# Performance work log

Measured on AMD Instinct MI355X. Metric: run time of the kernel, lower is better.

## Reference

```python
import jax, jax.numpy as jnp
import numpy as np

VOCAB = 32000
HID = 1024
HEADS = 16
HEAD_DIM = HID // HEADS
LAYERS = 8
INTER = 4 * HID
ROPE_BASE = 100000.0
EPS = 1e-5


def setup_inputs() -> dict:
    key = jax.random.key(0)
    ks = jax.random.split(key, 12)
    s = 0.02
    inp = {
        'input_ids': jax.random.randint(ks[0], (2, 2048), 0, VOCAB),
        'embed_W': jax.random.normal(ks[1], (VOCAB, HID), jnp.float32) * s,
        'Wq': jax.random.normal(ks[2], (LAYERS, HID, HID), jnp.float32) * s,
        'Wk': jax.random.normal(ks[3], (LAYERS, HID, HID), jnp.float32) * s,
        'Wv': jax.random.normal(ks[4], (LAYERS, HID, HID), jnp.float32) * s,
        'Wo': jax.random.normal(ks[5], (LAYERS, HID, HID), jnp.float32) * s,
        'Wg': jax.random.normal(ks[6], (LAYERS, HID, INTER), jnp.float32) * s,
        'Wu': jax.random.normal(ks[7], (LAYERS, HID, INTER), jnp.float32) * s,
        'Wd': jax.random.normal(ks[8], (LAYERS, INTER, HID), jnp.float32) * s,
        'norm1_w': jnp.ones((LAYERS, HID), jnp.float32),
        'norm2_w': jnp.ones((LAYERS, HID), jnp.float32),
        'final_norm_w': jnp.ones((HID,), jnp.float32),
        'head_W': jax.random.normal(ks[9], (HID, VOCAB), jnp.float32) * s,
    }
    return inp


def rms_norm(x, w):
    return x * jax.lax.rsqrt(jnp.mean(x * x, axis=-1, keepdims=True) + EPS) * w


def rope_tables(seq_len):
    freq = 1.0 / (ROPE_BASE ** (jnp.arange(0, HEAD_DIM, 2, dtype=jnp.float32) / HEAD_DIM))
    ang = jnp.arange(seq_len, dtype=jnp.float32)[:, None] * freq  # [S, d/2]
    cos = jnp.concatenate([jnp.cos(ang), jnp.cos(ang)], axis=-1)  # [S, d]
    sin = jnp.concatenate([jnp.sin(ang), jnp.sin(ang)], axis=-1)
    return cos, sin


def rotate_half(x):
    h = x.shape[-1] // 2
    return jnp.concatenate([-x[..., h:], x[..., :h]], axis=-1)


def apply_rope(q, k, cos, sin):
    # q,k: [B,S,H,D]; cos,sin: [S,D] -> broadcast over heads via [:,None,:]
    c = cos[:, None, :]
    s = sin[:, None, :]
    return q * c + rotate_half(q) * s, k * c + rotate_half(k) * s


def attention(x, wq, wk, wv, wo, cos, sin, causal_mask):
    B, S, _ = x.shape
    q = (x @ wq).reshape(B, S, HEADS, HEAD_DIM)
    k = (x @ wk).reshape(B, S, HEADS, HEAD_DIM)
    v = (x @ wv).reshape(B, S, HEADS, HEAD_DIM)
    q, k = apply_rope(q, k, cos, sin)
    scores = jnp.einsum('bqhd,bkhd->bhqk', q, k) / np.sqrt(HEAD_DIM)
    scores = jnp.clip(scores, -1000.0, 1000.0)
    scores = jnp.where(causal_mask, jnp.finfo(scores.dtype).min, scores)
    w = jax.nn.softmax(scores.astype(jnp.float32), axis=-1).astype(q.dtype)
    w = jnp.clip(w, 0.0, 1.0)
    ctx = jnp.einsum('bhqk,bkhd->bqhd', w, v).reshape(B, S, HID)
    return ctx @ wo


def reference(input_ids, embed_W, Wq, Wk, Wv, Wo, Wg, Wu, Wd, norm1_w, norm2_w, final_norm_w, head_W):
    B, S = input_ids.shape
    h = embed_W[input_ids]  # [B,S,HID]
    cos, sin = rope_tables(S)
    causal_mask = jnp.triu(jnp.ones((S, S), bool), k=1)[None, None]
    for l in range(LAYERS):
        h = h + attention(rms_norm(h, norm1_w[l]), Wq[l], Wk[l], Wv[l], Wo[l], cos, sin, causal_mask)
        hn = rms_norm(h, norm2_w[l])
        h = h + (jax.nn.silu(hn @ Wg[l]) * (hn @ Wu[l])) @ Wd[l]
    h = rms_norm(h, final_norm_w)
    logits = h @ head_W
    return logits, h
```

## Files before the change

### kernel.cpp

```cpp
#include <hip/hip_runtime.h>

#define T_TOK 4096
#define SEQ   2048
#define HID   1024
#define NH    16
#define HD    64
#define INTER 4096
#define NLAYER 8
#define VOCAB 32000

typedef short short8 __attribute__((ext_vector_type(8)));
typedef float f32x4  __attribute__((ext_vector_type(4)));

__device__ __forceinline__ unsigned short f2bf(float f){
  unsigned int u = __builtin_bit_cast(unsigned int, f);
  u += 0x7fffu + ((u >> 16) & 1u);
  return (unsigned short)(u >> 16);
}
__device__ __forceinline__ float bf2f(unsigned short b){
  unsigned int u = ((unsigned int)b) << 16;
  return __builtin_bit_cast(float, u);
}

#define GLOAD_LDS16(gsrc, ldst) \
  __builtin_amdgcn_global_load_lds((const __attribute__((address_space(1))) void*)(gsrc), \
                                   (__attribute__((address_space(3))) void*)(ldst), 16, 0, 0)

__global__ __launch_bounds__(256) void embed_kernel(const int* __restrict__ ids,
                                                    const float* __restrict__ W,
                                                    float* __restrict__ h){
  int i = blockIdx.x * 256 + threadIdx.x;
  int t = i >> 8, c = i & 255;
  ((float4*)h)[i] = ((const float4*)(W + (size_t)ids[t] * HID))[c];
}

__global__ __launch_bounds__(256) void rope_tab_kernel(float* __restrict__ cosT,
                                                       float* __restrict__ sinT){
  int i = blockIdx.x * 256 + threadIdx.x;
  int s = i >> 5, f = i & 31;
  float inv = expf(-((2.0f * (float)f) / 64.0f) * logf(100000.0f));
  float ang = (float)s * inv;
  cosT[i] = cosf(ang);
  sinT[i] = sinf(ang);
}

__global__ __launch_bounds__(256) void rmsnorm_kernel(const float* __restrict__ h,
                                                      const float* __restrict__ w,
                                                      unsigned short* __restrict__ out,
                                                      float* hcopy){
  int t = blockIdx.x, tid = threadIdx.x;
  float4 v = ((const float4*)(h + (size_t)t * HID))[tid];
  float ss = v.x*v.x + v.y*v.y + v.z*v.z + v.w*v.w;
  #pragma unroll
  for (int m = 1; m < 64; m <<= 1) ss += __shfl_xor(ss, m);
  __shared__ float red[4];
  if ((tid & 63) == 0) red[tid >> 6] = ss;
  __syncthreads();
  float r = rsqrtf((red[0] + red[1] + red[2] + red[3]) * (1.0f / HID) + 1e-5f);
  float4 wv = ((const float4*)w)[tid];
  float nx = v.x * r * wv.x;
  float ny = v.y * r * wv.y;
  float nz = v.z * r * wv.z;
  float nw = v.w * r * wv.w;
  ushort4 o;
  o.x = f2bf(nx); o.y = f2bf(ny); o.z = f2bf(nz); o.w = f2bf(nw);
  ((ushort4*)(out + (size_t)t * HID))[tid] = o;
  if (hcopy){
    float4 hv; hv.x = nx; hv.y = ny; hv.z = nz; hv.w = nw;
    ((float4*)(hcopy + (size_t)t * HID))[tid] = hv;
  }
}

__global__ __launch_bounds__(256) void convert_w_qkvo(const float* __restrict__ W0,
                                                      const float* __restrict__ W1,
                                                      const float* __restrict__ W2,
                                                      const float* __restrict__ W3,
                                                      unsigned short* __restrict__ Wt){
  __shared__ unsigned short t_lds[64][72];
  const int z = blockIdx.z, sel = z >> 3, l = z & 7;
  const float* W = ((sel == 0) ? W0 : (sel == 1) ? W1 : (sel == 2) ? W2 : W3)
                 + (size_t)l * HID * HID;
  unsigned short* dst = Wt + (size_t)z * HID * HID;
  const int n0 = blockIdx.x * 64, k0 = blockIdx.y * 64;
  const int tid = threadIdx.x;
  const int tr = tid >> 4, tc = tid & 15;
  #pragma unroll
  for (int i = 0; i < 4; ++i){
    int kk = tr + i * 16;
    float4 v = *(const float4*)(W + (size_t)(k0 + kk) * HID + n0 + tc * 4);
    t_lds[tc*4+0][kk] = f2bf(v.x);
    t_lds[tc*4+1][kk] = f2bf(v.y);
    t_lds[tc*4+2][kk] = f2bf(v.z);
    t_lds[tc*4+3][kk] = f2bf(v.w);
  }
  __syncthreads();
  const int n = tid >> 2, cp = tid & 3;
  #pragma unroll
  for (int j = 0; j < 2; ++j){
    int c = cp * 2 + j;
    uint4 d = *(const uint4*)(&t_lds[n][c * 8]);
    *(uint4*)(dst + (size_t)(n0 + n) * HID + k0 + ((c ^ (n & 7)) << 3)) = d;
  }
}

__global__ __launch_bounds__(256) void convert_w_swz(const float* __restrict__ W,
                                                     unsigned short* __restrict__ Wt,
                                                     int K, int N){
  __shared__ unsigned short t_lds[64][72];
  W  += (size_t)blockIdx.z * K * N;
  Wt += (size_t)blockIdx.z * K * N;
  const int n0 = blockIdx.x * 64, k0 = blockIdx.y * 64;
  const int tid = threadIdx.x;
  const int tr = tid >> 4, tc = tid & 15;
  #pragma unroll
  for (int i = 0; i < 4; ++i){
    int kk = tr + i * 16;
    float4 v = *(const float4*)(W + (size_t)(k0 + kk) * N + n0 + tc * 4);
    t_lds[tc*4+0][kk] = f2bf(v.x);
    t_lds[tc*4+1][kk] = f2bf(v.y);
    t_lds[tc*4+2][kk] = f2bf(v.z);
    t_lds[tc*4+3][kk] = f2bf(v.w);
  }
  __syncthreads();
  const int n = tid >> 2, cp = tid & 3;
  #pragma unroll
  for (int j = 0; j < 2; ++j){
    int c = cp * 2 + j;
    uint4 d = *(const uint4*)(&t_lds[n][c * 8]);
    *(uint4*)(Wt + (size_t)(n0 + n) * K + k0 + ((c ^ (n & 7)) << 3)) = d;
  }
}

__global__ __launch_bounds__(256) void convert_w_lin(const float* __restrict__ W,
                                                     unsigned short* __restrict__ Wt,
                                                     int K, int N){
  __shared__ unsigned short t_lds[64][72];
  const int n0 = blockIdx.x * 64, k0 = blockIdx.y * 64;
  const int tid = threadIdx.x;
  const int tr = tid >> 4, tc = tid & 15;
  #pragma unroll
  for (int i = 0; i < 4; ++i){
    int kk = tr + i * 16;
    float4 v = *(const float4*)(W + (size_t)(k0 + kk) * N + n0 + tc * 4);
    t_lds[tc*4+0][kk] = f2bf(v.x);
    t_lds[tc*4+1][kk] = f2bf(v.y);
    t_lds[tc*4+2][kk] = f2bf(v.z);
    t_lds[tc*4+3][kk] = f2bf(v.w);
  }
  __syncthreads();
  const int n = tid >> 2, cp = tid & 3;
  #pragma unroll
  for (int j = 0; j < 2; ++j){
    int c = cp * 2 + j;
    uint4 d = *(const uint4*)(&t_lds[n][c * 8]);
    *(uint4*)(Wt + (size_t)(n0 + n) * K + k0 + c * 8) = d;
  }
}

__device__ __forceinline__ void gemm_core64(const unsigned short* __restrict__ A,
                                            const unsigned short* __restrict__ Bt,
                                            int K, int m0, int n0,
                                            unsigned short* As, unsigned short* Bs,
                                            f32x4 (&acc)[4][4]){
  const int tid = threadIdx.x;
  const int lane = tid & 63, w = tid >> 6;
  const int l15 = lane & 15, g = lane >> 4;
  const int lr = lane >> 3;
  const int lc = lane & 7;
  const int wr = w >> 1, wc = w & 1;
  const int axor = ((lc ^ lr) << 3);

  #pragma unroll
  for (int m = 0; m < 4; ++m)
    #pragma unroll
    for (int n = 0; n < 4; ++n)
      #pragma unroll
      for (int i = 0; i < 4; ++i) acc[m][n][i] = 0.0f;

  for (int kk = 0; kk < K; kk += 64){
    __syncthreads();
    #pragma unroll
    for (int i = 0; i < 4; ++i){
      int rb = (i * 4 + w) * 8;
      GLOAD_LDS16(A  + (size_t)(m0 + rb + lr) * K + kk + axor,      As + rb * 64);
      GLOAD_LDS16(Bt + (size_t)(n0 + rb + lr) * K + kk + (lc << 3), Bs + rb * 64);
    }
    __syncthreads();
    short8 a[4][2], b[4][2];
    const int x = l15 & 7;
    #pragma unroll
    for (int m = 0; m < 4; ++m){
      int row = wr * 64 + m * 16 + l15;
      a[m][0] = *(const short8*)(As + row * 64 + ((g       ^ x) << 3));
      a[m][1] = *(const short8*)(As + row * 64 + (((4 + g) ^ x) << 3));
    }
    #pragma unroll
    for (int n = 0; n < 4; ++n){
      int row = wc * 64 + n * 16 + l15;
      b[n][0] = *(const short8*)(Bs + row * 64 + ((g       ^ x) << 3));
      b[n][1] = *(const short8*)(Bs + row * 64 + (((4 + g) ^ x) << 3));
    }
    #pragma unroll
    for (int m = 0; m < 4; ++m)
      #pragma unroll
      for (int n = 0; n < 4; ++n){
        acc[m][n] = __builtin_amdgcn_mfma_f32_16x16x32_bf16(a[m][0], b[n][0], acc[m][n], 0, 0, 0);
        acc[m][n] = __builtin_amdgcn_mfma_f32_16x16x32_bf16(a[m][1], b[n][1], acc[m][n], 0, 0, 0);
      }
  }
}

__device__ __forceinline__ void gemm_core32(const unsigned short* __restrict__ A,
                                            const unsigned short* __restrict__ Bt,
                                            int K, int m0, int n0,
                                            unsigned short* As, unsigned short* Bs,
                                            f32x4 (&acc)[4][4]){
  const int tid = threadIdx.x;
  const int lane = tid & 63, w = tid >> 6;
  const int l15 = lane & 15, g = lane >> 4;
  const int wr = w >> 1, wc = w & 1;
  const int srow = lane >> 2;
  const int schunk = (((lane & 3) ^ ((srow >> 1) & 3)) << 3);
  const int sx = (l15 >> 1) & 3;

  #pragma unroll
  for (int m = 0; m < 4; ++m)
    #pragma unroll
    for (int n = 0; n < 4; ++n)
      #pragma unroll
      for (int i = 0; i < 4; ++i) acc[m][n][i] = 0.0f;

  for (int kk = 0; kk < K; kk += 32){
    __syncthreads();
    GLOAD_LDS16(A  + (size_t)(m0 +      w*16 + srow) * K + kk + schunk, As + (w*16) * 32);
    GLOAD_LDS16(A  + (size_t)(m0 + 64 + w*16 + srow) * K + kk + schunk, As + (64 + w*16) * 32);
    GLOAD_LDS16(Bt + (size_t)(n0 +      w*16 + srow) * K + kk + schunk, Bs + (w*16) * 32);
    GLOAD_LDS16(Bt + (size_t)(n0 + 64 + w*16 + srow) * K + kk + schunk, Bs + (64 + w*16) * 32);
    __syncthreads();
    short8 a[4], b[4];
    #pragma unroll
    for (int m = 0; m < 4; ++m)
      a[m] = *(const short8*)(As + (wr*64 + m*16 + l15) * 32 + ((g ^ sx) << 3));
    #pragma unroll
    for (int n = 0; n < 4; ++n)
      b[n] = *(const short8*)(Bs + (wc*64 + n*16 + l15) * 32 + ((g ^ sx) << 3));
    #pragma unroll
    for (int m = 0; m < 4; ++m)
      #pragma unroll
      for (int n = 0; n < 4; ++n)
        acc[m][n] = __builtin_amdgcn_mfma_f32_16x16x32_bf16(a[m], b[n], acc[m][n], 0, 0, 0);
  }
}

template<int MODE>
__device__ __forceinline__ void gemm_epi(const f32x4 (&acc)[4][4], void* Cout,
                                         const float* __restrict__ resid,
                                         int N, int m0, int n0, int ldt){
  const int tid = threadIdx.x;
  const int lane = tid & 63, w = tid >> 6;
  const int l15 = lane & 15, g = lane >> 4;
  const int wr = w >> 1, wc = w & 1;
  #pragma unroll
  for (int m = 0; m < 4; ++m){
    #pragma unroll
    for (int n = 0; n < 4; ++n){
      int row0 = m0 + wr * 64 + m * 16 + g * 4;
      int col  = n0 + wc * 64 + n * 16 + l15;
      #pragma unroll
      for (int i = 0; i < 4; ++i){
        float v = acc[m][n][i];
        if (MODE == 0){
          ((unsigned short*)Cout)[(size_t)(row0 + i) * N + col] = f2bf(v);
        } else if (MODE == 1){
          size_t idx = (size_t)(row0 + i) * N + col;
          ((float*)Cout)[idx] = resid[idx] + v;
        } else if (MODE == 2){
          ((unsigned short*)Cout)[(size_t)col * ldt + (row0 + i)] = f2bf(v);
        } else {
          __builtin_nontemporal_store(v, &((float*)Cout)[(size_t)(row0 + i) * N + col]);
        }
      }
    }
  }
}

__global__ __launch_bounds__(256) void gemm_od(const unsigned short* __restrict__ A,
                                               const unsigned short* __restrict__ Bt,
                                               float* __restrict__ Cout,
                                               const float* __restrict__ resid,
                                               int K, int N){
  __shared__ unsigned short As[64 * 64];
  __shared__ unsigned short Bs[128 * 64];
  const int tid = threadIdx.x;
  const int lane = tid & 63, w = tid >> 6;
  const int l15 = lane & 15, g = lane >> 4;
  const int lr = lane >> 3, lc = lane & 7;
  const int axor = ((lc ^ lr) << 3);
  const int m0 = blockIdx.x * 64, n0 = blockIdx.y * 128;

  f32x4 acc[4][2];
  #pragma unroll
  for (int m = 0; m < 4; ++m)
    #pragma unroll
    for (int n = 0; n < 2; ++n)
      #pragma unroll
      for (int i = 0; i < 4; ++i) acc[m][n][i] = 0.0f;

  for (int kk = 0; kk < K; kk += 64){
    __syncthreads();
    #pragma unroll
    for (int i = 0; i < 2; ++i){
      int rb = (i * 4 + w) * 8;
      GLOAD_LDS16(A + (size_t)(m0 + rb + lr) * K + kk + axor, As + rb * 64);
    }
    #pragma unroll
    for (int i = 0; i < 4; ++i){
      int rb = (i * 4 + w) * 8;
      GLOAD_LDS16(Bt + (size_t)(n0 + rb + lr) * K + kk + (lc << 3), Bs + rb * 64);
    }
    __syncthreads();
    short8 a[4][2], b[2][2];
    const int x = l15 & 7;
    #pragma unroll
    for (int m = 0; m < 4; ++m){
      int row = m * 16 + l15;
      a[m][0] = *(const short8*)(As + row * 64 + ((g       ^ x) << 3));
      a[m][1] = *(const short8*)(As + row * 64 + (((4 + g) ^ x) << 3));
    }
    #pragma unroll
    for (int n = 0; n < 2; ++n){
      int row = w * 32 + n * 16 + l15;
      b[n][0] = *(const short8*)(Bs + row * 64 + ((g       ^ x) << 3));
      b[n][1] = *(const short8*)(Bs + row * 64 + (((4 + g) ^ x) << 3));
    }
    #pragma unroll
    for (int m = 0; m < 4; ++m)
      #pragma unroll
      for (int n = 0; n < 2; ++n){
        acc[m][n] = __builtin_amdgcn_mfma_f32_16x16x32_bf16(a[m][0], b[n][0], acc[m][n], 0, 0, 0);
        acc[m][n] = __builtin_amdgcn_mfma_f32_16x16x32_bf16(a[m][1], b[n][1], acc[m][n], 0, 0, 0);
      }
  }
  #pragma unroll
  for (int m = 0; m < 4; ++m)
    #pragma unroll
    for (int n = 0; n < 2; ++n){
      int row0 = m0 + m * 16 + g * 4;
      int col  = n0 + w * 32 + n * 16 + l15;
      #pragma unroll
      for (int i = 0; i < 4; ++i){
        size_t idx = (size_t)(row0 + i) * N + col;
        Cout[idx] = resid[idx] + acc[m][n][i];
      }
    }
}

template<int MODE>
__global__ __launch_bounds__(256) void gemm32_k(const unsigned short* __restrict__ A,
                                                const unsigned short* __restrict__ Bt,
                                                void* Cout, const float* resid,
                                                int K, int N, int ldt){
  __shared__ unsigned short As[128 * 32];
  __shared__ unsigned short Bs[128 * 32];
  f32x4 acc[4][4];
  gemm_core32(A, Bt, K, blockIdx.x * 128, blockIdx.y * 128, As, Bs, acc);
  gemm_epi<MODE>(acc, Cout, resid, N, blockIdx.x * 128, blockIdx.y * 128, ldt);
}

__global__ __launch_bounds__(256) void gemm_qkv(const unsigned short* __restrict__ A,
                                                const unsigned short* __restrict__ BtQ,
                                                const unsigned short* __restrict__ BtK,
                                                const unsigned short* __restrict__ BtV,
                                                unsigned short* qb, unsigned short* kb,
                                                unsigned short* vt,
                                                const float* __restrict__ cosT,
                                                const float* __restrict__ sinT){
  __shared__ unsigned short As[128 * 64];
  __shared__ unsigned short Bs[128 * 64];
  const int nb = blockIdx.y, sel = nb >> 3, n0 = (nb & 7) * 128;
  const unsigned short* Bt = (sel == 0) ? BtQ : (sel == 1) ? BtK : BtV;
  f32x4 acc[4][4];
  gemm_core64(A, Bt, HID, blockIdx.x * 128, n0, As, Bs, acc);
  if (sel == 2){
    gemm_epi<2>(acc, vt, nullptr, HID, blockIdx.x * 128, n0, T_TOK);
    return;
  }
  unsigned short* outp = sel ? kb : qb;
  const float qs = sel ? 1.0f : 0.125f;
  const int tid = threadIdx.x;
  const int lane = tid & 63, w = tid >> 6;
  const int l15 = lane & 15, g = lane >> 4;
  const int wr = w >> 1, wc = w & 1;
  const int m0 = blockIdx.x * 128;
  #pragma unroll
  for (int m = 0; m < 4; ++m){
    #pragma unroll
    for (int n = 0; n < 2; ++n){
      int row0 = m0 + wr * 64 + m * 16 + g * 4;
      int col  = n0 + wc * 64 + n * 16 + l15;
      int f    = (col & 63);
      #pragma unroll
      for (int i = 0; i < 4; ++i){
        int t = row0 + i, s = t & (SEQ - 1);
        float c  = cosT[s * 32 + f];
        float sn = sinT[s * 32 + f];
        float x0 = acc[m][n][i], x1 = acc[m][n + 2][i];
        outp[(size_t)t * HID + col]      = f2bf((x0 * c - x1 * sn) * qs);
        outp[(size_t)t * HID + col + 32] = f2bf((x1 * c + x0 * sn) * qs);
      }
    }
  }
}

__global__ __launch_bounds__(256) void gemm_gusilu(const unsigned short* __restrict__ A,
                                                   const unsigned short* __restrict__ BtG,
                                                   const unsigned short* __restrict__ BtU,
                                                   unsigned short* __restrict__ gb){
  __shared__ unsigned short As[128 * 64];
  __shared__ unsigned short Bs[128 * 64];
  const int m0 = blockIdx.x * 128, n0 = blockIdx.y * 128;
  f32x4 acc[4][4];
  gemm_core64(A, BtG, HID, m0, n0, As, Bs, acc);
  unsigned int gp[4][4][2];
  #pragma unroll
  for (int m = 0; m < 4; ++m)
    #pragma unroll
    for (int n = 0; n < 4; ++n){
      gp[m][n][0] = (unsigned int)f2bf(acc[m][n][0]) | ((unsigned int)f2bf(acc[m][n][1]) << 16);
      gp[m][n][1] = (unsigned int)f2bf(acc[m][n][2]) | ((unsigned int)f2bf(acc[m][n][3]) << 16);
    }
  gemm_core64(A, BtU, HID, m0, n0, As, Bs, acc);
  const int tid = threadIdx.x;
  const int lane = tid & 63, w = tid >> 6;
  const int l15 = lane & 15, g = lane >> 4;
  const int wr = w >> 1, wc = w & 1;
  #pragma unroll
  for (int m = 0; m < 4; ++m){
    #pragma unroll
    for (int n = 0; n < 4; ++n){
      int row0 = m0 + wr * 64 + m * 16 + g * 4;
      int col  = n0 + wc * 64 + n * 16 + l15;
      #pragma unroll
      for (int i = 0; i < 4; ++i){
        float gv = bf2f((unsigned short)(gp[m][n][i >> 1] >> ((i & 1) * 16)));
        float u  = acc[m][n][i];
        float s  = (gv / (1.0f + __expf(-gv))) * u;
        gb[(size_t)(row0 + i) * INTER + col] = f2bf(s);
      }
    }
  }
}

__global__ __launch_bounds__(256, 2) void gemm_f32b(const unsigned short* __restrict__ A,
                                                    const float* __restrict__ Bw,
                                                    float* __restrict__ Cout,
                                                    int M, int N, int K){
  __shared__ unsigned short As[128 * 32];
  __shared__ unsigned short Bs[128 * 32];
  const int tid = threadIdx.x;
  const int lane = tid & 63, wid = tid >> 6;
  const int l15 = lane & 15, g = lane >> 4;
  const int wr = wid >> 1, wc = wid & 1;
  const int m0 = blockIdx.x * 128, n0 = blockIdx.y * 128;
  const int bcol = tid & 127, bhalf = tid >> 7;
  f32x4 acc[4][4];
  #pragma unroll
  for (int m = 0; m < 4; ++m)
    #pragma unroll
    for (int n = 0; n < 4; ++n)
      #pragma unroll
      for (int i = 0; i < 4; ++i) acc[m][n][i] = 0.0f;
  for (int kk = 0; kk < K; kk += 32){
    __syncthreads();
    #pragma unroll
    for (int cc = 0; cc < 2; ++cc){
      int c = tid + cc * 256;
      int row = c >> 2, kc = (c & 3) << 3;
      uint4 d = *(const uint4*)(A + (size_t)(m0 + row) * K + kk + kc);
      *(uint4*)(&As[row * 32 + kc]) = d;
    }
    {
      const float* bp = Bw + (size_t)(kk + bhalf * 16) * N + n0 + bcol;
      float f[16];
      #pragma unroll
      for (int j = 0; j < 16; ++j) f[j] = bp[(size_t)j * N];
      unsigned int pk[8];
      #pragma unroll
      for (int j = 0; j < 8; ++j)
        pk[j] = (unsigned int)f2bf(f[2*j]) | ((unsigned int)f2bf(f[2*j+1]) << 16);
      int sw = (bcol >> 1) & 3;
      int c0 = ((bhalf << 1)     ) ^ sw;
      int c1 = ((bhalf << 1) | 1 ) ^ sw;
      uint4 w0; w0.x = pk[0]; w0.y = pk[1]; w0.z = pk[2]; w0.w = pk[3];
      uint4 w1; w1.x = pk[4]; w1.y = pk[5]; w1.z = pk[6]; w1.w = pk[7];
      *(uint4*)(&Bs[bcol * 32 + c0 * 8]) = w0;
      *(uint4*)(&Bs[bcol * 32 + c1 * 8]) = w1;
    }
    __syncthreads();
    short8 a[4], b[4];
    #pragma unroll
    for (int m = 0; m < 4; ++m)
      a[m] = *(const short8*)(&As[(wr*64 + m*16 + l15) * 32 + g*8]);
    #pragma unroll
    for (int n = 0; n < 4; ++n){
      int col = wc*64 + n*16 + l15;
      b[n] = *(const short8*)(&Bs[col * 32 + (g ^ ((col >> 1) & 3)) * 8]);
    }
    #pragma unroll
    for (int m = 0; m < 4; ++m)
      #pragma unroll
      for (int n = 0; n < 4; ++n)
        acc[m][n] = __builtin_amdgcn_mfma_f32_16x16x32_bf16(a[m], b[n], acc[m][n], 0, 0, 0);
  }
  #pragma unroll
  for (int m = 0; m < 4; ++m)
    #pragma unroll
    for (int n = 0; n < 4; ++n){
      int row0 = m0 + wr*64 + m*16 + g*4;
      int col  = n0 + wc*64 + n*16 + l15;
      #pragma unroll
      for (int i = 0; i < 4; ++i)
        Cout[(size_t)(row0 + i) * N + col] = acc[m][n][i];
    }
}

__global__ __launch_bounds__(512) void attn_kernel(const unsigned short* __restrict__ q,
                                                   const unsigned short* __restrict__ k,
                                                   const unsigned short* __restrict__ vt,
                                                   unsigned short* __restrict__ ctx){
  const int tid = threadIdx.x;
  const int lane = tid & 63, w = tid >> 6;
  const int l15 = lane & 15, g = lane >> 4;
  const int bx = (int)gridDim.x - 1 - (int)blockIdx.x;
  const int q0 = bx * 128 + w * 16;
  const int hh = blockIdx.y;
  const int tb = blockIdx.z * SEQ;

  __shared__ unsigned short Ks[64][72];
  __shared__ unsigned short Vs[64][72];
  __shared__ unsigned short Ps[8][16][72];

  short8 qa[2];
  #pragma unroll
  for (int kd = 0; kd < 2; ++kd)
    qa[kd] = *(const short8*)(q + (size_t)(tb + q0 + l15) * HID + hh*HD + kd*32 + g*8);

  float m_run[4], l_run[4];
  f32x4 o_acc[4];
  #pragma unroll
  for (int i = 0; i < 4; ++i){ m_run[i] = -1e30f; l_run[i] = 0.0f; }
  #pragma unroll
  for (int dt = 0; dt < 4; ++dt)
    #pragma unroll
    for (int i = 0; i < 4; ++i) o_acc[dt][i] = 0.0f;

  const int ntile = 2 * bx + 2;
  const int srow = tid >> 3, sc = (tid & 7) * 8;
  const unsigned short* kbase = k  + (size_t)(tb + srow) * HID + hh*HD + sc;
  const unsigned short* vbase = vt + (size_t)(hh*HD + srow) * T_TOK + tb + sc;

  for (int kt = 0; kt < ntile; ++kt){
    const int kv0 = kt * 64;
    __syncthreads();
    *(uint4*)(&Ks[srow][sc]) = *(const uint4*)(kbase + (size_t)kv0 * HID);
    *(uint4*)(&Vs[srow][sc]) = *(const uint4*)(vbase + kv0);
    __syncthreads();
    const int dq = q0 + 15 - kv0;
    const int nct = (dq < 0) ? 0 : min(4, (dq >> 4) + 1);
    if (nct <= 0) continue;

    float pv[4][4];
    #pragma unroll
    for (int ct = 0; ct < 4; ++ct){
      if (ct < nct){
        f32x4 scv;
        #pragma unroll
        for (int i = 0; i < 4; ++i) scv[i] = 0.0f;
        scv = __builtin_amdgcn_mfma_f32_16x16x32_bf16(qa[0],
                *(const short8*)(&Ks[ct*16 + l15][g*8]), scv, 0, 0, 0);
        scv = __builtin_amdgcn_mfma_f32_16x16x32_bf16(qa[1],
                *(const short8*)(&Ks[ct*16 + l15][32 + g*8]), scv, 0, 0, 0);
        #pragma unroll
        for (int i = 0; i < 4; ++i){
          float s = fminf(fmaxf(scv[i], -1000.0f), 1000.0f);
          int row = q0 + g*4 + i;
          int col = kv0 + ct*16 + l15;
          pv[ct][i] = (col > row) ? -1e30f : s;
        }
      } else {
        #pragma unroll
        for (int i = 0; i < 4; ++i) pv[ct][i] = -1e30f;
      }
    }
    #pragma unroll
    for (int i = 0; i < 4; ++i){
      float mx = fmaxf(fmaxf(pv[0][i], pv[1][i]), fmaxf(pv[2][i], pv[3][i]));
      #pragma unroll
      for (int msk = 1; msk < 16; msk <<= 1) mx = fmaxf(mx, __shfl_xor(mx, msk));
      if (!__all(mx <= m_run[i] + 8.0f)){
        float mnew = fmaxf(m_run[i], mx);
        float scale = __expf(m_run[i] - mnew);
        m_run[i] = mnew;
        l_run[i] *= scale;
        #pragma unroll
        for (int dt = 0; dt < 4; ++dt) o_acc[dt][i] *= scale;
      }
      float psum = 0.0f;
      #pragma unroll
      for (int ct = 0; ct < 4; ++ct){
        if (ct < nct){
          float p = __expf(pv[ct][i] - m_run[i]);
          pv[ct][i] = p; psum += p;
        } else pv[ct][i] = 0.0f;
      }
      #pragma unroll
      for (int msk = 1; msk < 16; msk <<= 1) psum += __shfl_xor(psum, msk);
      l_run[i] += psum;
    }
    #pragma unroll
    for (int ct = 0; ct < 4; ++ct)
      #pragma unroll
      for (int i = 0; i < 4; ++i)
        Ps[w][g*4 + i][ct*16 + l15] = f2bf(pv[ct][i]);
    const int nks = (nct + 1) >> 1;
    #pragma unroll
    for (int ks = 0; ks < 2; ++ks){
      if (ks < nks){
        short8 ap = *(const short8*)(&Ps[w][l15][ks*32 + g*8]);
        #pragma unroll
        for (int dt = 0; dt < 4; ++dt){
          short8 vb = *(const short8*)(&Vs[dt*16 + l15][ks*32 + g*8]);
          o_acc[dt] = __builtin_amdgcn_mfma_f32_16x16x32_bf16(ap, vb, o_acc[dt], 0, 0, 0);
        }
      }
    }
  }
  #pragma unroll
  for (int i = 0; i < 4; ++i) l_run[i] = 1.0f / l_run[i];
  #pragma unroll
  for (int dt = 0; dt < 4; ++dt)
    #pragma unroll
    for (int i = 0; i < 4; ++i){
      float o = o_acc[dt][i] * l_run[i];
      ctx[(size_t)(tb + q0 + g*4 + i) * HID + hh*HD + dt*16 + l15] = f2bf(o);
    }
}

extern "C" void kernel_launch(void* const* d_in, const int* in_sizes, int n_in,
                              void* d_out, int out_size, void* d_ws, size_t ws_size,
                              hipStream_t stream){
  const int*   ids    = (const int*)d_in[0];
  const float* embedW = (const float*)d_in[1];
  const float* Wq = (const float*)d_in[2];
  const float* Wk = (const float*)d_in[3];
  const float* Wv = (const float*)d_in[4];
  const float* Wo = (const float*)d_in[5];
  const float* Wg = (const float*)d_in[6];
  const float* Wu = (const float*)d_in[7];
  const float* Wd = (const float*)d_in[8];
  const float* n1 = (const float*)d_in[9];
  const float* n2 = (const float*)d_in[10];
  const float* nf = (const float*)d_in[11];
  const float* Wh = (const float*)d_in[12];
  float* out = (float*)d_out;

  char* scb = (char*)d_out;
  unsigned short* qb  = (unsigned short*)(scb + 0);
  unsigned short* kb  = (unsigned short*)(scb + 8388608);
  unsigned short* vtb = (unsigned short*)(scb + 16777216);
  unsigned short* ctx = (unsigned short*)(scb + 25165824);
  unsigned short* gb  = (unsigned short*)(scb + 33554432);
  float* cosT = (float*)(scb + 100663296);
  float* sinT = (float*)(scb + 100925440);
  float* h_fallback   = (float*)(scb + 104857600);
  unsigned short* WtQ = (unsigned short*)(scb + 134217728);
  unsigned short* WtK = (unsigned short*)(scb + 150994944);
  unsigned short* WtV = (unsigned short*)(scb + 167772160);
  unsigned short* WtO = (unsigned short*)(scb + 184549376);
  unsigned short* WtG = (unsigned short*)(scb + 201326592);
  unsigned short* WtU = (unsigned short*)(scb + 268435456);
  unsigned short* WtD = (unsigned short*)(scb + 335544320);

  unsigned short* xn = (unsigned short*)d_ws;
  float* h = (ws_size >= 25165824u) ? (float*)((char*)d_ws + 8388608) : h_fallback;
  unsigned short* WhT = (ws_size >= 90701824u)
                      ? (unsigned short*)((char*)d_ws + 25165824) : nullptr;

  convert_w_qkvo<<<dim3(16, 16, 32), 256, 0, stream>>>(Wq, Wk, Wv, Wo, WtQ);
  convert_w_swz<<<dim3(64, 16, 8), 256, 0, stream>>>(Wg, WtG, HID, INTER);
  convert_w_swz<<<dim3(64, 16, 8), 256, 0, stream>>>(Wu, WtU, HID, INTER);
  convert_w_swz<<<dim3(16, 64, 8), 256, 0, stream>>>(Wd, WtD, INTER, HID);
  if (WhT)
    convert_w_lin<<<dim3(500, 16, 1), 256, 0, stream>>>(Wh, WhT, HID, VOCAB);

  embed_kernel<<<4096, 256, 0, stream>>>(ids, embedW, h);
  rope_tab_kernel<<<256, 256, 0, stream>>>(cosT, sinT);

  for (int l = 0; l < NLAYER; ++l){
    rmsnorm_kernel<<<4096, 256, 0, stream>>>(h, n1 + l*HID, xn, nullptr);
    gemm_qkv<<<dim3(32, 24), 256, 0, stream>>>(xn, WtQ + (size_t)l*HID*HID,
                                               WtK + (size_t)l*HID*HID,
                                               WtV + (size_t)l*HID*HID, qb, kb, vtb,
                                               cosT, sinT);
    attn_kernel<<<dim3(16, 16, 2), 512, 0, stream>>>(qb, kb, vtb, ctx);
    gemm_od<<<dim3(64, 8), 256, 0, stream>>>(ctx, WtO + (size_t)l*HID*HID,
                                             h, h, HID, HID);
    rmsnorm_kernel<<<4096, 256, 0, stream>>>(h, n2 + l*HID, xn, nullptr);
    gemm_gusilu<<<dim3(32, 32), 256, 0, stream>>>(xn, WtG + (size_t)l*HID*INTER,
                                                  WtU + (size_t)l*HID*INTER, gb);
    gemm_od<<<dim3(64, 8), 256, 0, stream>>>(gb, WtD + (size_t)l*HID*INTER,
                                             h, h, INTER, HID);
  }

  rmsnorm_kernel<<<4096, 256, 0, stream>>>(h, nf, xn, out + 131072000);
  if (WhT)
    gemm32_k<3><<<dim3(32, 250), 256, 0, stream>>>(xn, WhT, out, nullptr, HID, VOCAB, 0);
  else
    gemm_f32b<<<dim3(32, 250), 256, 0, stream>>>(xn, Wh, out, T_TOK, VOCAB, HID);
}
```

Baseline: 3.700 ms.

## Replace LM-head GEMM with 256x256 double-buffered 8-wave pipelined kernel

The vocabulary projection GEMM moves from a 128x128 tile, K=32, single-buffered kernel to a 256x256 tile kernel with 512 threads and K=64 stages. The new kernel double-buffers LDS, splits each stage into quarter-tile loads interleaved with MFMA phases, uses explicit vmcnt waits and s_setprio, and writes logits with nontemporal stores. The aim is to overlap global loads with compute and raise reuse per loaded byte on the largest GEMM. In exchange it uses 128KB of LDS, more registers and hand-tuned barrier ordering, which could limit occupancy or introduce races.

```diff
diff --git a/kernel.cpp b/kernel.cpp
--- a/kernel.cpp
+++ b/kernel.cpp
@@ -210,48 +210,6 @@
   }
 }
 
-__device__ __forceinline__ void gemm_core32(const unsigned short* __restrict__ A,
-                                            const unsigned short* __restrict__ Bt,
-                                            int K, int m0, int n0,
-                                            unsigned short* As, unsigned short* Bs,
-                                            f32x4 (&acc)[4][4]){
-  const int tid = threadIdx.x;
-  const int lane = tid & 63, w = tid >> 6;
-  const int l15 = lane & 15, g = lane >> 4;
-  const int wr = w >> 1, wc = w & 1;
-  const int srow = lane >> 2;
-  const int schunk = (((lane & 3) ^ ((srow >> 1) & 3)) << 3);
-  const int sx = (l15 >> 1) & 3;
-
-  #pragma unroll
-  for (int m = 0; m < 4; ++m)
-    #pragma unroll
-    for (int n = 0; n < 4; ++n)
-      #pragma unroll
-      for (int i = 0; i < 4; ++i) acc[m][n][i] = 0.0f;
-
-  for (int kk = 0; kk < K; kk += 32){
-    __syncthreads();
-    GLOAD_LDS16(A  + (size_t)(m0 +      w*16 + srow) * K + kk + schunk, As + (w*16) * 32);
-    GLOAD_LDS16(A  + (size_t)(m0 + 64 + w*16 + srow) * K + kk + schunk, As + (64 + w*16) * 32);
-    GLOAD_LDS16(Bt + (size_t)(n0 +      w*16 + srow) * K + kk + schunk, Bs + (w*16) * 32);
-    GLOAD_LDS16(Bt + (size_t)(n0 + 64 + w*16 + srow) * K + kk + schunk, Bs + (64 + w*16) * 32);
-    __syncthreads();
-    short8 a[4], b[4];
-    #pragma unroll
-    for (int m = 0; m < 4; ++m)
-      a[m] = *(const short8*)(As + (wr*64 + m*16 + l15) * 32 + ((g ^ sx) << 3));
-    #pragma unroll
-    for (int n = 0; n < 4; ++n)
-      b[n] = *(const short8*)(Bs + (wc*64 + n*16 + l15) * 32 + ((g ^ sx) << 3));
-    #pragma unroll
-    for (int m = 0; m < 4; ++m)
-      #pragma unroll
-      for (int n = 0; n < 4; ++n)
-        acc[m][n] = __builtin_amdgcn_mfma_f32_16x16x32_bf16(a[m], b[n], acc[m][n], 0, 0, 0);
-  }
-}
-
 template<int MODE>
 __device__ __forceinline__ void gemm_epi(const f32x4 (&acc)[4][4], void* Cout,
                                          const float* __restrict__ resid,
@@ -355,16 +313,157 @@
     }
 }
 
-template<int MODE>
-__global__ __launch_bounds__(256) void gemm32_k(const unsigned short* __restrict__ A,
-                                                const unsigned short* __restrict__ Bt,
-                                                void* Cout, const float* resid,
-                                                int K, int N, int ldt){
-  __shared__ unsigned short As[128 * 32];
-  __shared__ unsigned short Bs[128 * 32];
-  f32x4 acc[4][4];
-  gemm_core32(A, Bt, K, blockIdx.x * 128, blockIdx.y * 128, As, Bs, acc);
-  gemm_epi<MODE>(acc, Cout, resid, N, blockIdx.x * 128, blockIdx.y * 128, ldt);
+#define WAITV4 asm volatile("s_waitcnt vmcnt(4)" ::: "memory")
+#define WAITV2 asm volatile("s_waitcnt vmcnt(2)" ::: "memory")
+#define WAITV0 asm volatile("s_waitcnt vmcnt(0)" ::: "memory")
+#define HBAR() { __builtin_amdgcn_s_barrier(); asm volatile("" ::: "memory"); }
+
+__global__ __launch_bounds__(512, 2) void gemm_head8p(const unsigned short* __restrict__ A,
+                                                      const unsigned short* __restrict__ Bt,
+                                                      float* __restrict__ out){
+  __shared__ unsigned short smem8[65536];
+  const int tid = threadIdx.x;
+  const int lane = tid & 63, w = tid >> 6;
+  const int l15 = lane & 15, g = lane >> 4;
+  const int wr = w >> 2, wc = w & 3;
+  const int lr8 = lane >> 3, lc = lane & 7;
+  const int axor = ((lc ^ lr8) << 3);
+  const int x = l15 & 7;
+  const int sl0 = ((g ^ x) << 3), sl1 = (((4 + g) ^ x) << 3);
+  const int m0 = blockIdx.x * 256, n0 = blockIdx.y * 256;
+  const int K = HID, nt = HID / 64;
+
+  f32x4 acc[8][4];
+  #pragma unroll
+  for (int m = 0; m < 8; ++m)
+    #pragma unroll
+    for (int n = 0; n < 4; ++n)
+      #pragma unroll
+      for (int i = 0; i < 4; ++i) acc[m][n][i] = 0.0f;
+
+  #define STAGE_HALF(BUF, MAT, HALF, KK)                                           \
+  {                                                                                \
+    unsigned short* dbase = smem8 + ((((BUF)*2+(MAT))*2+(HALF)) << 13) + (w*8)*64; \
+    const unsigned short* G = (MAT) ? Bt : A;                                      \
+    const int brc = (MAT) ? n0 : m0;                                               \
+    int r0 = w*8 + lr8, r1 = r0 + 64;                                              \
+    int g0, g1;                                                                    \
+    if (MAT){ g0 = brc + ((r0>>5)<<6) + ((HALF)<<5) + (r0&31);                     \
+              g1 = brc + ((r1>>5)<<6) + ((HALF)<<5) + (r1&31); }                   \
+    else    { g0 = brc + ((r0>>6)<<7) + ((HALF)<<6) + (r0&63);                     \
+              g1 = brc + ((r1>>6)<<7) + ((HALF)<<6) + (r1&63); }                   \
+    GLOAD_LDS16(G + (size_t)g0*K + (KK) + axor, dbase);                            \
+    GLOAD_LDS16(G + (size_t)g1*K + (KK) + axor, dbase + 64*64);                    \
+  }
+
+  STAGE_HALF(0, 0, 0, 0)
+  STAGE_HALF(0, 1, 0, 0)
+  STAGE_HALF(0, 1, 1, 0)
+  STAGE_HALF(0, 0, 1, 0)
+  WAITV4;
+  HBAR();
+
+  for (int t = 0; t < nt; ++t){
+    const int buf = t & 1, sb = buf ^ 1;
+    const int kkn = (t + 1) * 64;
+    const bool st = (t + 1 < nt);
+    const int aB0 = ((buf*2+0)*2+0) << 13;
+    const int aB1 = aB0 + 8192;
+    const int bB0 = ((buf*2+1)*2+0) << 13;
+    const int bB1 = bB0 + 8192;
+    short8 a[4][2], b0[2][2], b1[2][2];
+
+    #pragma unroll
+    for (int m4 = 0; m4 < 4; ++m4){
+      const unsigned short* p = smem8 + aB0 + (wr*64 + m4*16 + l15) * 64;
+      a[m4][0] = *(const short8*)(p + sl0);
+      a[m4][1] = *(const short8*)(p + sl1);
+    }
+    #pragma unroll
+    for (int n2 = 0; n2 < 2; ++n2){
+      const unsigned short* p = smem8 + bB0 + (wc*32 + n2*16 + l15) * 64;
+      b0[n2][0] = *(const short8*)(p + sl0);
+      b0[n2][1] = *(const short8*)(p + sl1);
+    }
+    if (st){ STAGE_HALF(sb, 0, 0, kkn) }
+    HBAR();
+    __builtin_amdgcn_s_setprio(1);
+    #pragma unroll
+    for (int m4 = 0; m4 < 4; ++m4)
+      #pragma unroll
+      for (int n2 = 0; n2 < 2; ++n2){
+        acc[m4][n2] = __builtin_amdgcn_mfma_f32_16x16x32_bf16(a[m4][0], b0[n2][0], acc[m4][n2], 0, 0, 0);
+        acc[m4][n2] = __builtin_amdgcn_mfma_f32_16x16x32_bf16(a[m4][1], b0[n2][1], acc[m4][n2], 0, 0, 0);
+      }
+    __builtin_amdgcn_s_setprio(0);
+    if (st){ WAITV4; } else { WAITV2; }
+    HBAR();
+
+    #pragma unroll
+    for (int n2 = 0; n2 < 2; ++n2){
+      const unsigned short* p = smem8 + bB1 + (wc*32 + n2*16 + l15) * 64;
+      b1[n2][0] = *(const short8*)(p + sl0);
+      b1[n2][1] = *(const short8*)(p + sl1);
+    }
+    if (st){ STAGE_HALF(sb, 1, 0, kkn) }
+    HBAR();
+    __builtin_amdgcn_s_setprio(1);
+    #pragma unroll
+    for (int m4 = 0; m4 < 4; ++m4)
+      #pragma unroll
+      for (int n2 = 0; n2 < 2; ++n2){
+        acc[m4][2+n2] = __builtin_amdgcn_mfma_f32_16x16x32_bf16(a[m4][0], b1[n2][0], acc[m4][2+n2], 0, 0, 0);
+        acc[m4][2+n2] = __builtin_amdgcn_mfma_f32_16x16x32_bf16(a[m4][1], b1[n2][1], acc[m4][2+n2], 0, 0, 0);
+      }
+    __builtin_amdgcn_s_setprio(0);
+    if (st){ WAITV4; } else { WAITV0; }
+    HBAR();
+
+    #pragma unroll
+    for (int m4 = 0; m4 < 4; ++m4){
+      const unsigned short* p = smem8 + aB1 + (wr*64 + m4*16 + l15) * 64;
+      a[m4][0] = *(const short8*)(p + sl0);
+      a[m4][1] = *(const short8*)(p + sl1);
+    }
+    if (st){ STAGE_HALF(sb, 1, 1, kkn) }
+    HBAR();
+    __builtin_amdgcn_s_setprio(1);
+    #pragma unroll
+    for (int m4 = 0; m4 < 4; ++m4)
+      #pragma unroll
+      for (int n2 = 0; n2 < 2; ++n2){
+        acc[4+m4][n2] = __builtin_amdgcn_mfma_f32_16x16x32_bf16(a[m4][0], b0[n2][0], acc[4+m4][n2], 0, 0, 0);
+        acc[4+m4][n2] = __builtin_amdgcn_mfma_f32_16x16x32_bf16(a[m4][1], b0[n2][1], acc[4+m4][n2], 0, 0, 0);
+      }
+    __builtin_amdgcn_s_setprio(0);
+    HBAR();
+
+    if (st){ STAGE_HALF(sb, 0, 1, kkn) }
+    HBAR();
+    __builtin_amdgcn_s_setprio(1);
+    #pragma unroll
+    for (int m4 = 0; m4 < 4; ++m4)
+      #pragma unroll
+      for (int n2 = 0; n2 < 2; ++n2){
+        acc[4+m4][2+n2] = __builtin_amdgcn_mfma_f32_16x16x32_bf16(a[m4][0], b1[n2][0], acc[4+m4][2+n2], 0, 0, 0);
+        acc[4+m4][2+n2] = __builtin_amdgcn_mfma_f32_16x16x32_bf16(a[m4][1], b1[n2][1], acc[4+m4][2+n2], 0, 0, 0);
+      }
+    __builtin_amdgcn_s_setprio(0);
+    if (st){ WAITV4; }
+    HBAR();
+  }
+  #undef STAGE_HALF
+
+  #pragma unroll
+  for (int m = 0; m < 8; ++m)
+    #pragma unroll
+    for (int n = 0; n < 4; ++n){
+      int row0 = m0 + wr*128 + m*16 + g*4;
+      int col  = n0 + wc*64  + n*16 + l15;
+      #pragma unroll
+      for (int i = 0; i < 4; ++i)
+        __builtin_nontemporal_store(acc[m][n][i], &out[(size_t)(row0 + i) * VOCAB + col]);
+    }
 }
 
 __global__ __launch_bounds__(256) void gemm_qkv(const unsigned short* __restrict__ A,
@@ -714,7 +813,7 @@
 
   rmsnorm_kernel<<<4096, 256, 0, stream>>>(h, nf, xn, out + 131072000);
   if (WhT)
-    gemm32_k<3><<<dim3(32, 250), 256, 0, stream>>>(xn, WhT, out, nullptr, HID, VOCAB, 0);
+    gemm_head8p<<<dim3(16, 125), 512, 0, stream>>>(xn, WhT, out);
   else
     gemm_f32b<<<dim3(32, 250), 256, 0, stream>>>(xn, Wh, out, T_TOK, VOCAB, HID);
 }
```

After: 3.644 ms (median of 2 runs). About the same (-1.5%).
